# Kernel tuning notes

Measured on AMD Instinct MI355X. Metric: run time of the kernel, lower is better.

The kernel has to match this reference:

```python
import jax, jax.numpy as jnp
import numpy as np

DIM = 384
HEADS = 8
HD = DIM // HEADS
GAMMA = 0.5
EPS = 1e-6
BN_EPS = 1e-5
LN_EPS = 1e-5


def setup_inputs() -> dict:
    key = jax.random.key(0)
    ks = jax.random.split(key, 8)
    B, H, W = 8, 56, 56
    d = DIM
    w = lambda k, shp: (jax.random.normal(k, shp, jnp.float32) * 0.05)
    return {
        "x": jax.random.normal(ks[0], (B, d, H, W), jnp.float32),
        "bn1_w": jnp.ones((d,), jnp.float32), "bn1_b": jnp.zeros((d,), jnp.float32),
        "bn1_m": jnp.zeros((d,), jnp.float32), "bn1_v": jnp.ones((d,), jnp.float32),
        "cw1": w(ks[1], (d, d)), "cb1": jnp.zeros((d,), jnp.float32),
        "dw": w(ks[2], (d, 1, 3, 3)), "db": jnp.zeros((d,), jnp.float32),
        "bn2_w": jnp.ones((d,), jnp.float32), "bn2_b": jnp.zeros((d,), jnp.float32),
        "bn2_m": jnp.zeros((d,), jnp.float32), "bn2_v": jnp.ones((d,), jnp.float32),
        "cw2": w(ks[3], (d, d)), "cb2": jnp.zeros((d,), jnp.float32),
        "qkv_w": w(ks[4], (3 * d, d)),
        "proj_w": w(ks[5], (d, d)), "proj_b": jnp.zeros((d,), jnp.float32),
        "ln_w": jnp.ones((d,), jnp.float32), "ln_b": jnp.zeros((d,), jnp.float32),
        "mlp_w1": w(ks[6], (d, 4 * d)), "mlp_b1": jnp.zeros((4 * d,), jnp.float32),
        "mlp_w2": w(ks[7], (4 * d, d)), "mlp_b2": jnp.zeros((d,), jnp.float32),
    }


def _bn(t, w, b, m, v):
    # inference-mode BatchNorm2d over channel dim of NCHW
    s = w * jax.lax.rsqrt(v + BN_EPS)
    return (t - m[:, None, None]) * s[:, None, None] + b[:, None, None]


def _c1(t, w, b=None):
    # 1x1 conv as channel GEMM: (o,i) x (b,i,h,w) -> (b,o,h,w)
    y = jnp.einsum('oi,bihw->bohw', w, t)
    return y if b is None else y + b[:, None, None]


def _phi(t):
    return jnp.exp(GAMMA * (2.0 * t - t * t))


def reference(x, bn1_w, bn1_b, bn1_m, bn1_v, cw1, cb1, dw, db,
              bn2_w, bn2_b, bn2_m, bn2_v, cw2, cb2, qkv_w,
              proj_w, proj_b, ln_w, ln_b, mlp_w1, mlp_b1, mlp_w2, mlp_b2):
    B, C, H, W = x.shape
    N = H * W
    # conv_path with residual
    h = _bn(x, bn1_w, bn1_b, bn1_m, bn1_v)
    h = _c1(h, cw1, cb1)
    h = jax.lax.conv_general_dilated(h, dw, (1, 1), 'SAME',
                                     feature_group_count=DIM,
                                     dimension_numbers=('NCHW', 'OIHW', 'NCHW'))
    h = h + db[:, None, None]
    h = _bn(h, bn2_w, bn2_b, bn2_m, bn2_v)
    h = _c1(h, cw2, cb2)
    x1 = h + x
    # linear attention
    qkv = _c1(x1, qkv_w)  # (B, 3C, H, W)
    q, k, v = jnp.split(qkv, 3, axis=1)
    to_heads = lambda t: t.reshape(B, HEADS, HD, N).transpose(0, 1, 3, 2)  # (B,h,N,d)
    qp = _phi(to_heads(q))
    kp = _phi(to_heads(k))
    vv = to_heads(v)
    kv = jnp.einsum('bhnd,bhne->bhde', kp, vv)               # (B,h,d,d)
    z = 1.0 / (jnp.einsum('bhnd,bhd->bhn', qp, kp.sum(axis=2)) + EPS)
    out = jnp.einsum('bhnd,bhde->bhne', qp, kv) * z[..., None]  # (B,h,N,d)
    out = out.transpose(0, 1, 3, 2).reshape(B, C, H, W)
    out = _c1(out, proj_w, proj_b)
    x2 = x1 + out
    # LayerNorm + MLP over channels
    xf = x2.transpose(0, 2, 3, 1)  # (B,H,W,C)
    mu = xf.mean(-1, keepdims=True)
    var = xf.var(-1, keepdims=True)
    xn = (xf - mu) * jax.lax.rsqrt(var + LN_EPS) * ln_w + ln_b
    hmid = jax.nn.gelu(xn @ mlp_w1 + mlp_b1, approximate=False)
    mlp_out = hmid @ mlp_w2 + mlp_b2
    return x2 + mlp_out.transpose(0, 3, 1, 2)
```

## Files before the change

### kernel.cpp

```cpp
#include <hip/hip_runtime.h>

#define CDIM 384
#define NPIX 3136
#define BB 8
#define NROW (BB * NPIX)
#define HDIM 48
#define CMID 1536
#define BN_EPS 1e-5f
#define LN_EPS 1e-5f

typedef short s16x8 __attribute__((ext_vector_type(8)));
typedef float f32x4 __attribute__((ext_vector_type(4)));
typedef unsigned short u16;

__device__ __forceinline__ u16 f2bf(float f) {
    unsigned u = __builtin_bit_cast(unsigned, f);
    u = (u + 0x7FFFu + ((u >> 16) & 1u)) >> 16;
    return (u16)u;
}
__device__ __forceinline__ float bf2f(u16 h) {
    unsigned u = ((unsigned)h) << 16;
    return __builtin_bit_cast(float, u);
}
__device__ __forceinline__ float phi_act(float v) { return expf(0.5f * (2.f * v - v * v)); }
__device__ __forceinline__ float gelu_act(float v) { return 0.5f * v * (1.f + erff(v * 0.7071067811865476f)); }

#define GLL16(g, l) __builtin_amdgcn_global_load_lds( \
    (const __attribute__((address_space(1))) void*)(g), \
    (__attribute__((address_space(3))) void*)(l), 16, 0, 0)

template<int ACT, bool BIAS, bool RES, bool OBF, bool OF32, int TN, bool QKV>
__global__ __launch_bounds__(256) void gemm_mfma(
    const u16* __restrict__ A, const u16* __restrict__ Bw,
    u16* __restrict__ Cbf, u16* __restrict__ Cv, float* __restrict__ Cf,
    const float* __restrict__ res, const float* __restrict__ bias,
    int N, int K)
{
    constexpr int NFR = TN / 32;
    constexpr int TNw = TN / 2;
    constexpr int STR = TNw + 4;
    constexpr int KLOOP_U16 = 8192 + TN * 64;
    constexpr int STG_U16 = 4 * 64 * STR;
    constexpr int SMEM_N = KLOOP_U16 > STG_U16 ? KLOOP_U16 : STG_U16;
    __shared__ __align__(16) u16 smem[SMEM_N];
    u16* Asb = smem;
    u16* Bsb = smem + 8192;

    const int t  = threadIdx.x;
    const int wv = t >> 6, ln = t & 63;
    const int lm = ln & 15, lq = ln >> 4;
    const int wm = wv >> 1, wn = wv & 1;
    const int m0 = blockIdx.y << 7, n0 = blockIdx.x * TN;

    const u16* gA0 = A  + (long)(m0 + wv * 16 + lm) * K + lq * 8;
    const u16* gA1 = gA0 + (long)64 * K;
    const u16* gB0 = Bw + (long)(n0 + wv * 16 + lm) * K + lq * 8;
    const u16* gB1 = gB0 + (long)64 * K;

    f32x4 acc[4][NFR] = {};
    const int nk = K >> 5;

    GLL16(gA0, &Asb[wv * 512]);
    GLL16(gA1, &Asb[wv * 512 + 2048]);
    GLL16(gB0, &Bsb[wv * 512]);
    if constexpr (TN == 128) GLL16(gB1, &Bsb[wv * 512 + 2048]);

    for (int k = 0; k < nk; k++) {
        const int cur = k & 1;
        __syncthreads();
        if (k + 1 < nk) {
            const int nx = cur ^ 1;
            gA0 += 32; gA1 += 32; gB0 += 32;
            GLL16(gA0, &Asb[nx * 4096 + wv * 512]);
            GLL16(gA1, &Asb[nx * 4096 + wv * 512 + 2048]);
            GLL16(gB0, &Bsb[nx * TN * 32 + wv * 512]);
            if constexpr (TN == 128) { gB1 += 32; GLL16(gB1, &Bsb[nx * TN * 32 + wv * 512 + 2048]); }
        }
        s16x8 av[4], bv[NFR];
        #pragma unroll
        for (int mf = 0; mf < 4; mf++)
            av[mf] = *(const s16x8*)&Asb[cur * 4096 + (wm * 256 + mf * 64 + ln) * 8];
        #pragma unroll
        for (int nf = 0; nf < NFR; nf++)
            bv[nf] = *(const s16x8*)&Bsb[cur * TN * 32 + ((TN == 128 ? wn * 256 : wn * 128) + nf * 64 + ln) * 8];
        #pragma unroll
        for (int mf = 0; mf < 4; mf++)
            #pragma unroll
            for (int nf = 0; nf < NFR; nf++)
                acc[mf][nf] = __builtin_amdgcn_mfma_f32_16x16x32_bf16(
                    av[mf], bv[nf], acc[mf][nf], 0, 0, 0);
    }

    u16* obase = Cbf; int oldc = N; int ocol0 = n0;
    bool qk_phi = false;
    if constexpr (QKV) {
        if (n0 < 768) { obase = Cbf; oldc = 768; ocol0 = n0; qk_phi = true; }
        else          { obase = Cv;  oldc = 384; ocol0 = n0 - 768; }
    }

    if constexpr (OBF || QKV) {
        __syncthreads();
        u16* stg = smem + wv * (64 * STR);
        #pragma unroll
        for (int nf = 0; nf < NFR; nf++) {
            const int lc = nf * 16 + lm;
            const int gn = n0 + wn * TNw + lc;
            const float bval = BIAS ? bias[gn] : 0.f;
            #pragma unroll
            for (int mf = 0; mf < 4; mf++) {
                #pragma unroll
                for (int r = 0; r < 4; r++) {
                    const int lr = mf * 16 + lq * 4 + r;
                    float v = acc[mf][nf][r];
                    if (BIAS) v += bval;
                    if (ACT == 1) v = phi_act(v);
                    else if (ACT == 2) v = gelu_act(v);
                    if (QKV) { if (qk_phi) v = phi_act(v); }
                    const long off = (long)(m0 + wm * 64 + lr) * N + gn;
                    if (RES) v += res[off];
                    if (OF32) Cf[off] = v;
                    stg[lr * STR + lc] = f2bf(v);
                }
            }
        }
        __syncthreads();
        constexpr int CPR = TNw / 8;
        constexpr int RPI = 64 / CPR;
        const int cg = ln % CPR, rb = ln / CPR;
        #pragma unroll
        for (int it = 0; it < 64 / RPI; it++) {
            const int row = it * RPI + rb;
            const s16x8 vv = *(const s16x8*)&stg[row * STR + cg * 8];
            *(s16x8*)&obase[(long)(m0 + wm * 64 + row) * oldc + ocol0 + wn * TNw + cg * 8] = vv;
        }
    } else {
        #pragma unroll
        for (int nf = 0; nf < NFR; nf++) {
            const int gn = n0 + wn * TNw + nf * 16 + lm;
            const float bval = BIAS ? bias[gn] : 0.f;
            #pragma unroll
            for (int mf = 0; mf < 4; mf++) {
                const int gmb = m0 + wm * 64 + mf * 16 + lq * 4;
                #pragma unroll
                for (int r = 0; r < 4; r++) {
                    float v = acc[mf][nf][r];
                    if (BIAS) v += bval;
                    if (ACT == 1) v = phi_act(v);
                    else if (ACT == 2) v = gelu_act(v);
                    const long off = (long)(gmb + r) * N + gn;
                    if (RES) v += res[off];
                    Cf[off] = v;
                }
            }
        }
    }
}

__global__ __launch_bounds__(256) void nchw_to_nhwc(const float* __restrict__ x,
                                                    float* __restrict__ of,
                                                    u16* __restrict__ ob)
{
    __shared__ float tile[64 * 65];
    const int n0 = blockIdx.x << 6, c0 = blockIdx.y << 6, b = blockIdx.z;
    const int t = threadIdx.x;
    const float* ip = x + ((long)b * CDIM + c0) * NPIX + n0;
    for (int idx = t; idx < 4096; idx += 256) {
        const int cc = idx >> 6, nn = idx & 63;
        tile[cc * 65 + nn] = ip[(long)cc * NPIX + nn];
    }
    __syncthreads();
    for (int idx = t; idx < 4096; idx += 256) {
        const int nn = idx >> 6, cc = idx & 63;
        const float v = tile[cc * 65 + nn];
        const long o = ((long)b * NPIX + n0 + nn) * CDIM + c0 + cc;
        of[o] = v; ob[o] = f2bf(v);
    }
}

__global__ __launch_bounds__(256) void dwconv_nhwc(const u16* __restrict__ in,
                                                   const u16* __restrict__ wt,
                                                   u16* __restrict__ out)
{
    const long tid = (long)blockIdx.x * 256 + threadIdx.x;
    const int c8 = (int)(tid % 48);
    const int p  = (int)((tid / 48) % NPIX);
    const int b  = (int)(tid / (48LL * NPIX));
    const int y = p / 56, x = p % 56;
    const u16* base = in + (long)b * NPIX * CDIM + c8 * 8;
    float acc[8] = {};
    #pragma unroll
    for (int r = 0; r < 3; r++) {
        const int yy = y + r - 1;
        if ((unsigned)yy >= 56u) continue;
        #pragma unroll
        for (int s = 0; s < 3; s++) {
            const int xx = x + s - 1;
            if ((unsigned)xx >= 56u) continue;
            const s16x8 iv = *(const s16x8*)&base[(long)(yy * 56 + xx) * CDIM];
            const s16x8 wv = *(const s16x8*)&wt[(r * 3 + s) * CDIM + c8 * 8];
            #pragma unroll
            for (int j = 0; j < 8; j++)
                acc[j] = fmaf(bf2f((u16)iv[j]), bf2f((u16)wv[j]), acc[j]);
        }
    }
    s16x8 ov;
    #pragma unroll
    for (int j = 0; j < 8; j++) ov[j] = (short)f2bf(acc[j]);
    *(s16x8*)&out[((long)b * NPIX + p) * CDIM + c8 * 8] = ov;
}

__global__ __launch_bounds__(256) void attn_kv_k(const u16* __restrict__ qk,
                                                 const u16* __restrict__ vb,
                                                 float* __restrict__ kv,
                                                 float* __restrict__ ksum)
{
    const int sp = blockIdx.x, bh = blockIdx.y;
    const int b = bh >> 3, h = bh & 7;
    const u16* kbase = qk + (long)b * NPIX * 768 + 384 + h * HDIM;
    const u16* vbase = vb + (long)b * NPIX * CDIM + h * HDIM;
    __shared__ float kt[64 * 48];
    __shared__ float vt[64 * 48];
    const int t = threadIdx.x;
    const int dg = t >> 4, eg = t & 15;
    float acc[3][3] = {};
    float ks[3] = {};
    for (int tl = sp; tl < 49; tl += 8) {
        const int n0 = tl << 6;
        __syncthreads();
        for (int idx = t; idx < 3072; idx += 256) {
            const int nn = idx / 48, d = idx % 48;
            kt[idx] = bf2f(kbase[(long)(n0 + nn) * 768 + d]);
            vt[idx] = bf2f(vbase[(long)(n0 + nn) * CDIM + d]);
        }
        __syncthreads();
        for (int nn = 0; nn < 64; nn++) {
            float kvv[3], vvv[3];
            #pragma unroll
            for (int i = 0; i < 3; i++) kvv[i] = kt[nn * 48 + dg * 3 + i];
            #pragma unroll
            for (int j = 0; j < 3; j++) vvv[j] = vt[nn * 48 + eg * 3 + j];
            #pragma unroll
            for (int i = 0; i < 3; i++)
                #pragma unroll
                for (int j = 0; j < 3; j++)
                    acc[i][j] = fmaf(kvv[i], vvv[j], acc[i][j]);
            if (eg == 0) {
                #pragma unroll
                for (int i = 0; i < 3; i++) ks[i] += kvv[i];
            }
        }
    }
    float* kvp = kv + (long)bh * HDIM * HDIM;
    #pragma unroll
    for (int i = 0; i < 3; i++)
        #pragma unroll
        for (int j = 0; j < 3; j++)
            atomicAdd(&kvp[(dg * 3 + i) * HDIM + eg * 3 + j], acc[i][j]);
    if (eg == 0) {
        #pragma unroll
        for (int i = 0; i < 3; i++) atomicAdd(&ksum[bh * HDIM + dg * 3 + i], ks[i]);
    }
}

__global__ __launch_bounds__(256) void attn_out_k(const u16* __restrict__ qk,
                                                  const float* __restrict__ kv,
                                                  const float* __restrict__ ksum,
                                                  u16* __restrict__ outb)
{
    const int bh = blockIdx.y, b = bh >> 3, h = bh & 7;
    const int n0 = blockIdx.x << 6;
    const u16* qbase = qk + (long)b * NPIX * 768 + h * HDIM;
    __shared__ float qt[64 * 48];
    __shared__ float kvs[48 * 48];
    __shared__ float kss[48];
    const int t = threadIdx.x;
    for (int idx = t; idx < 3072; idx += 256) {
        const int nn = idx / 48, d = idx % 48;
        qt[idx] = bf2f(qbase[(long)(n0 + nn) * 768 + d]);
    }
    for (int idx = t; idx < 2304; idx += 256) kvs[idx] = kv[(long)bh * HDIM * HDIM + idx];
    if (t < 48) kss[t] = ksum[bh * HDIM + t];
    __syncthreads();
    const int nn = t & 63, eg = t >> 6;
    float a[12] = {};
    float dot = 0.f;
    for (int d = 0; d < 48; d++) {
        const float qd = qt[nn * 48 + d];
        dot = fmaf(qd, kss[d], dot);
        const float* kr = &kvs[d * 48 + eg * 12];
        #pragma unroll
        for (int e = 0; e < 12; e++) a[e] = fmaf(qd, kr[e], a[e]);
    }
    const float z = 1.f / (dot + 1e-6f);
    u16* op = outb + ((long)b * NPIX + n0 + nn) * CDIM + h * HDIM + eg * 12;
    #pragma unroll
    for (int e = 0; e < 12; e++) op[e] = f2bf(a[e] * z);
}

__global__ __launch_bounds__(256) void ln_k(const float* __restrict__ x2,
                                            const float* __restrict__ lw,
                                            const float* __restrict__ lb,
                                            u16* __restrict__ xn)
{
    const int row = blockIdx.x * 4 + (threadIdx.x >> 6);
    const int lane = threadIdx.x & 63;
    const float* rp = x2 + (long)row * CDIM;
    float2 v[3];
    float sum = 0.f, sq = 0.f;
    #pragma unroll
    for (int i = 0; i < 3; i++) {
        v[i] = *(const float2*)&rp[lane * 2 + i * 128];
        sum += v[i].x + v[i].y;
        sq = fmaf(v[i].x, v[i].x, fmaf(v[i].y, v[i].y, sq));
    }
    #pragma unroll
    for (int off = 1; off < 64; off <<= 1) {
        sum += __shfl_xor(sum, off);
        sq  += __shfl_xor(sq, off);
    }
    const float mu = sum * (1.f / CDIM);
    const float rs = rsqrtf(sq * (1.f / CDIM) - mu * mu + LN_EPS);
    u16* op = xn + (long)row * CDIM;
    #pragma unroll
    for (int i = 0; i < 3; i++) {
        const int c = lane * 2 + i * 128;
        op[c]     = f2bf((v[i].x - mu) * rs * lw[c] + lb[c]);
        op[c + 1] = f2bf((v[i].y - mu) * rs * lw[c + 1] + lb[c + 1]);
    }
}

__global__ __launch_bounds__(256) void final_out(const float* __restrict__ x2,
                                                 const float* __restrict__ mlp,
                                                 float* __restrict__ out)
{
    __shared__ float tile[64 * 65];
    const int n0 = blockIdx.x << 6, c0 = blockIdx.y << 6, b = blockIdx.z;
    const int t = threadIdx.x;
    for (int idx = t; idx < 4096; idx += 256) {
        const int nn = idx >> 6, cc = idx & 63;
        const long o = ((long)b * NPIX + n0 + nn) * CDIM + c0 + cc;
        tile[nn * 65 + cc] = x2[o] + mlp[o];
    }
    __syncthreads();
    float* op = out + ((long)b * CDIM + c0) * NPIX + n0;
    for (int idx = t; idx < 4096; idx += 256) {
        const int cc = idx >> 6, nn = idx & 63;
        op[(long)cc * NPIX + nn] = tile[nn * 65 + cc];
    }
}

__global__ void prep_bn_k(const float* __restrict__ w1, const float* __restrict__ b1,
                          const float* __restrict__ m1, const float* __restrict__ v1,
                          const float* __restrict__ w2, const float* __restrict__ b2,
                          const float* __restrict__ m2, const float* __restrict__ v2,
                          const float* __restrict__ db,
                          float* s1, float* t1, float* s2, float* t2)
{
    const int i = threadIdx.x;
    if (i < CDIM) {
        const float a = w1[i] * rsqrtf(v1[i] + BN_EPS);
        s1[i] = a; t1[i] = b1[i] - m1[i] * a;
        const float c = w2[i] * rsqrtf(v2[i] + BN_EPS);
        s2[i] = c; t2[i] = b2[i] - m2[i] * c + db[i] * c;
    }
}

__global__ __launch_bounds__(64) void prep_w_k(
    const float* __restrict__ cw1, const float* __restrict__ cb1,
    const float* __restrict__ cw2, const float* __restrict__ cb2,
    const float* __restrict__ s1, const float* __restrict__ t1,
    const float* __restrict__ s2, const float* __restrict__ t2,
    u16* __restrict__ w1e, float* __restrict__ b1e,
    u16* __restrict__ w2e, float* __restrict__ b2e)
{
    const int o = blockIdx.x;
    const bool sec = (o >= CDIM);
    const int oo = sec ? o - CDIM : o;
    const float* cw = sec ? cw2 : cw1;
    const float* cb = sec ? cb2 : cb1;
    const float* s  = sec ? s2  : s1;
    const float* tt = sec ? t2  : t1;
    u16* we = sec ? w2e : w1e;
    float* be = sec ? b2e : b1e;
    float part = 0.f;
    for (int i = threadIdx.x; i < CDIM; i += 64) {
        const float wv = cw[oo * CDIM + i];
        we[oo * CDIM + i] = f2bf(wv * s[i]);
        part += wv * tt[i];
    }
    for (int off = 32; off; off >>= 1) part += __shfl_down(part, off);
    if (threadIdx.x == 0) be[oo] = cb[oo] + part;
}

__global__ void cvt_k(const float* __restrict__ in, u16* __restrict__ out, int n)
{
    const int i = blockIdx.x * 256 + threadIdx.x;
    if (i < n) out[i] = f2bf(in[i]);
}

__global__ __launch_bounds__(256) void transcvt_k(const float* __restrict__ in,
                                                  u16* __restrict__ out, int R, int C)
{
    __shared__ float tile[64 * 65];
    const int c0 = blockIdx.x << 6, r0 = blockIdx.y << 6;
    const int t = threadIdx.x;
    for (int idx = t; idx < 4096; idx += 256) {
        const int rr = idx >> 6, cc = idx & 63;
        tile[rr * 65 + cc] = in[(long)(r0 + rr) * C + c0 + cc];
    }
    __syncthreads();
    for (int idx = t; idx < 4096; idx += 256) {
        const int cc = idx >> 6, rr = idx & 63;
        out[(long)(c0 + cc) * R + r0 + rr] = f2bf(tile[rr * 65 + cc]);
    }
}

__global__ void dwt_k(const float* __restrict__ dw, u16* __restrict__ o)
{
    const int i = blockIdx.x * 256 + threadIdx.x;
    if (i < 9 * CDIM) {
        const int c = i / 9, tap = i % 9;
        o[tap * CDIM + c] = f2bf(dw[i]);
    }
}

extern "C" void kernel_launch(void* const* d_in, const int* in_sizes, int n_in,
                              void* d_out, int out_size, void* d_ws, size_t ws_size,
                              hipStream_t stream)
{
    const float* x      = (const float*)d_in[0];
    const float* bn1_w  = (const float*)d_in[1];
    const float* bn1_b  = (const float*)d_in[2];
    const float* bn1_m  = (const float*)d_in[3];
    const float* bn1_v  = (const float*)d_in[4];
    const float* cw1    = (const float*)d_in[5];
    const float* cb1    = (const float*)d_in[6];
    const float* dwW    = (const float*)d_in[7];
    const float* db     = (const float*)d_in[8];
    const float* bn2_w  = (const float*)d_in[9];
    const float* bn2_b  = (const float*)d_in[10];
    const float* bn2_m  = (const float*)d_in[11];
    const float* bn2_v  = (const float*)d_in[12];
    const float* cw2    = (const float*)d_in[13];
    const float* cb2    = (const float*)d_in[14];
    const float* qkv_w  = (const float*)d_in[15];
    const float* proj_w = (const float*)d_in[16];
    const float* proj_b = (const float*)d_in[17];
    const float* ln_w   = (const float*)d_in[18];
    const float* ln_b   = (const float*)d_in[19];
    const float* mlp_w1 = (const float*)d_in[20];
    const float* mlp_b1 = (const float*)d_in[21];
    const float* mlp_w2 = (const float*)d_in[22];
    const float* mlp_b2 = (const float*)d_in[23];
    float* outF = (float*)d_out;

    const long S = (long)NROW * CDIM;
    float* wsf = (float*)d_ws;

    float* xh_f  = wsf;
    float* x2_f  = wsf;
    u16*   v_bf  = (u16*)wsf;
    float* x1_f  = wsf + S;
    u16*   hmid  = (u16*)(wsf + S);
    u16* ar   = (u16*)(wsf + 2 * S);
    u16* a0   = ar;
    u16* a1   = ar + S;
    u16* a2   = ar + 2 * S;
    float* mlp_f = (float*)(ar + S);
    u16* wtb   = (u16*)(wsf + 3 * S + S / 2);
    u16* w1e   = wtb;
    u16* w2e   = w1e + CDIM * CDIM;
    u16* qkvw  = w2e + CDIM * CDIM;
    u16* projw = qkvw + 1152 * CDIM;
    u16* mw1t  = projw + CDIM * CDIM;
    u16* mw2t  = mw1t + CMID * CDIM;
    u16* dwt   = mw2t + CDIM * CMID;
    float* fb  = (float*)(dwt + 9 * CDIM);
    float* b1e = fb;
    float* b2e = b1e + CDIM;
    float* s1  = b2e + CDIM;
    float* t1  = s1 + CDIM;
    float* s2  = t1 + CDIM;
    float* t2  = s2 + CDIM;
    float* kvb = t2 + CDIM;
    float* ksb = kvb + 64 * HDIM * HDIM;

    prep_bn_k<<<1, CDIM, 0, stream>>>(bn1_w, bn1_b, bn1_m, bn1_v,
                                      bn2_w, bn2_b, bn2_m, bn2_v, db, s1, t1, s2, t2);
    prep_w_k<<<2 * CDIM, 64, 0, stream>>>(cw1, cb1, cw2, cb2, s1, t1, s2, t2,
                                          w1e, b1e, w2e, b2e);
    cvt_k<<<(1152 * CDIM + 255) / 256, 256, 0, stream>>>(qkv_w, qkvw, 1152 * CDIM);
    cvt_k<<<(CDIM * CDIM + 255) / 256, 256, 0, stream>>>(proj_w, projw, CDIM * CDIM);
    transcvt_k<<<dim3(CMID / 64, CDIM / 64), 256, 0, stream>>>(mlp_w1, mw1t, CDIM, CMID);
    transcvt_k<<<dim3(CDIM / 64, CMID / 64), 256, 0, stream>>>(mlp_w2, mw2t, CMID, CDIM);
    dwt_k<<<(9 * CDIM + 255) / 256, 256, 0, stream>>>(dwW, dwt);

    nchw_to_nhwc<<<dim3(49, 6, 8), 256, 0, stream>>>(x, xh_f, a0);
    gemm_mfma<0, true, false, true, false, 64, false><<<dim3(6, 196), 256, 0, stream>>>(
        a0, w1e, a1, nullptr, nullptr, nullptr, b1e, CDIM, CDIM);
    dwconv_nhwc<<<(int)((long)BB * NPIX * 48 / 256), 256, 0, stream>>>(a1, dwt, a2);
    gemm_mfma<0, true, true, true, true, 64, false><<<dim3(6, 196), 256, 0, stream>>>(
        a2, w2e, a0, nullptr, x1_f, xh_f, b2e, CDIM, CDIM);
    gemm_mfma<0, false, false, true, false, 128, true><<<dim3(9, 196), 256, 0, stream>>>(
        a0, qkvw, a1, v_bf, nullptr, nullptr, nullptr, 1152, CDIM);
    hipMemsetAsync(kvb, 0, (size_t)(64 * HDIM * HDIM + 64 * HDIM) * sizeof(float), stream);
    attn_kv_k<<<dim3(8, 64), 256, 0, stream>>>(a1, v_bf, kvb, ksb);
    attn_out_k<<<dim3(49, 64), 256, 0, stream>>>(a1, kvb, ksb, a0);
    gemm_mfma<0, true, true, false, true, 64, false><<<dim3(6, 196), 256, 0, stream>>>(
        a0, projw, nullptr, nullptr, x2_f, x1_f, proj_b, CDIM, CDIM);
    ln_k<<<NROW / 4, 256, 0, stream>>>(x2_f, ln_w, ln_b, a0);
    const long RH = (long)NROW / 2;
    gemm_mfma<2, true, false, true, false, 128, false><<<dim3(12, 98), 256, 0, stream>>>(
        a0, mw1t, hmid, nullptr, nullptr, nullptr, mlp_b1, CMID, CDIM);
    gemm_mfma<0, true, false, false, true, 64, false><<<dim3(6, 98), 256, 0, stream>>>(
        hmid, mw2t, nullptr, nullptr, mlp_f, nullptr, mlp_b2, CDIM, CMID);
    gemm_mfma<2, true, false, true, false, 128, false><<<dim3(12, 98), 256, 0, stream>>>(
        a0 + RH * CDIM, mw1t, hmid, nullptr, nullptr, nullptr, mlp_b1, CMID, CDIM);
    gemm_mfma<0, true, false, false, true, 64, false><<<dim3(6, 98), 256, 0, stream>>>(
        hmid, mw2t, nullptr, nullptr, mlp_f + RH * CDIM, nullptr, mlp_b2, CDIM, CMID);
    final_out<<<dim3(49, 6, 8), 256, 0, stream>>>(x2_f, mlp_f, outF);
}
```

Before: 686.8 us.

## Move linear-attention KV and output contractions onto bf16 MFMA

Rewrites the attention K^T V reduction and the Q·KV output stage to use 16x16x32 bf16 MFMA instructions instead of scalar fp32 FMAs. The key sum is computed with an MFMA against a ones vector, and a new repack kernel converts KV and ksum to a padded, transposed bf16 layout. The output kernel stages results in LDS so it can issue coalesced vector stores. This cuts ALU work in the attention stages but adds a kernel launch and rounds KV to bf16, which may reduce accuracy.

```diff
diff --git a/kernel.cpp b/kernel.cpp
--- a/kernel.cpp
+++ b/kernel.cpp
@@ -209,7 +209,7 @@
     *(s16x8*)&out[((long)b * NPIX + p) * CDIM + c8 * 8] = ov;
 }
 
-__global__ __launch_bounds__(256) void attn_kv_k(const u16* __restrict__ qk,
+__global__ __launch_bounds__(256) void attn_kv_m(const u16* __restrict__ qk,
                                                  const u16* __restrict__ vb,
                                                  float* __restrict__ kv,
                                                  float* __restrict__ ksum)
@@ -218,83 +218,147 @@
     const int b = bh >> 3, h = bh & 7;
     const u16* kbase = qk + (long)b * NPIX * 768 + 384 + h * HDIM;
     const u16* vbase = vb + (long)b * NPIX * CDIM + h * HDIM;
-    __shared__ float kt[64 * 48];
-    __shared__ float vt[64 * 48];
+    __shared__ u16 kt[48 * 72];
+    __shared__ u16 vt[48 * 72];
     const int t = threadIdx.x;
-    const int dg = t >> 4, eg = t & 15;
-    float acc[3][3] = {};
-    float ks[3] = {};
+    const int wv = t >> 6, ln = t & 63, lm = ln & 15, lq = ln >> 4;
+
+    f32x4 acc[3] = {};
+    const s16x8 ones = {0x3F80, 0x3F80, 0x3F80, 0x3F80, 0x3F80, 0x3F80, 0x3F80, 0x3F80};
+
     for (int tl = sp; tl < 49; tl += 8) {
-        const int n0 = tl << 6;
+        const int nn0 = tl << 6;
         __syncthreads();
-        for (int idx = t; idx < 3072; idx += 256) {
-            const int nn = idx / 48, d = idx % 48;
-            kt[idx] = bf2f(kbase[(long)(n0 + nn) * 768 + d]);
-            vt[idx] = bf2f(vbase[(long)(n0 + nn) * CDIM + d]);
+        for (int idx = t; idx < 384; idx += 256) {
+            const int oct = idx >> 6, nn = idx & 63;
+            const s16x8 kvv = *(const s16x8*)&kbase[(long)(nn0 + nn) * 768 + oct * 8];
+            const s16x8 vvv = *(const s16x8*)&vbase[(long)(nn0 + nn) * CDIM + oct * 8];
+            #pragma unroll
+            for (int j = 0; j < 8; j++) {
+                kt[(oct * 8 + j) * 72 + nn] = (u16)kvv[j];
+                vt[(oct * 8 + j) * 72 + nn] = (u16)vvv[j];
+            }
         }
         __syncthreads();
-        for (int nn = 0; nn < 64; nn++) {
-            float kvv[3], vvv[3];
-            #pragma unroll
-            for (int i = 0; i < 3; i++) kvv[i] = kt[nn * 48 + dg * 3 + i];
-            #pragma unroll
-            for (int j = 0; j < 3; j++) vvv[j] = vt[nn * 48 + eg * 3 + j];
-            #pragma unroll
-            for (int i = 0; i < 3; i++)
+        #pragma unroll
+        for (int s = 0; s < 2; s++) {
+            if (wv < 3) {
+                const s16x8 av = *(const s16x8*)&kt[(wv * 16 + lm) * 72 + s * 32 + lq * 8];
                 #pragma unroll
-                for (int j = 0; j < 3; j++)
-                    acc[i][j] = fmaf(kvv[i], vvv[j], acc[i][j]);
-            if (eg == 0) {
+                for (int ef = 0; ef < 3; ef++) {
+                    const s16x8 bv = *(const s16x8*)&vt[(ef * 16 + lm) * 72 + s * 32 + lq * 8];
+                    acc[ef] = __builtin_amdgcn_mfma_f32_16x16x32_bf16(av, bv, acc[ef], 0, 0, 0);
+                }
+            } else {
                 #pragma unroll
-                for (int i = 0; i < 3; i++) ks[i] += kvv[i];
+                for (int mf = 0; mf < 3; mf++) {
+                    const s16x8 av = *(const s16x8*)&kt[(mf * 16 + lm) * 72 + s * 32 + lq * 8];
+                    acc[mf] = __builtin_amdgcn_mfma_f32_16x16x32_bf16(av, ones, acc[mf], 0, 0, 0);
+                }
             }
         }
     }
-    float* kvp = kv + (long)bh * HDIM * HDIM;
-    #pragma unroll
-    for (int i = 0; i < 3; i++)
-        #pragma unroll
-        for (int j = 0; j < 3; j++)
-            atomicAdd(&kvp[(dg * 3 + i) * HDIM + eg * 3 + j], acc[i][j]);
-    if (eg == 0) {
-        #pragma unroll
-        for (int i = 0; i < 3; i++) atomicAdd(&ksum[bh * HDIM + dg * 3 + i], ks[i]);
-    }
-}
-
-__global__ __launch_bounds__(256) void attn_out_k(const u16* __restrict__ qk,
-                                                  const float* __restrict__ kv,
-                                                  const float* __restrict__ ksum,
+    if (wv < 3) {
+        #pragma unroll
+        for (int ef = 0; ef < 3; ef++)
+            #pragma unroll
+            for (int r = 0; r < 4; r++)
+                atomicAdd(&kv[(long)bh * 2304 + (wv * 16 + lq * 4 + r) * 48 + ef * 16 + lm], acc[ef][r]);
+    } else {
+        if (lm == 0) {
+            #pragma unroll
+            for (int mf = 0; mf < 3; mf++)
+                #pragma unroll
+                for (int r = 0; r < 4; r++)
+                    atomicAdd(&ksum[bh * 48 + mf * 16 + lq * 4 + r], acc[mf][r]);
+        }
+    }
+}
+
+__global__ void repack_kv(const float* __restrict__ kvb, const float* __restrict__ ksb,
+                          u16* __restrict__ kvp, u16* __restrict__ ksp)
+{
+    const int bh = blockIdx.x, t = threadIdx.x;
+    for (int idx = t; idx < 3072; idx += 256) {
+        const int e = idx >> 6, d = idx & 63;
+        kvp[(long)bh * 3072 + idx] = (d < 48) ? f2bf(kvb[(long)bh * 2304 + d * 48 + e]) : (u16)0;
+    }
+    if (t < 64) ksp[bh * 64 + t] = (t < 48) ? f2bf(ksb[bh * 48 + t]) : (u16)0;
+}
+
+__global__ __launch_bounds__(256) void attn_out_m(const u16* __restrict__ qk,
+                                                  const u16* __restrict__ kvp,
+                                                  const u16* __restrict__ ksp,
                                                   u16* __restrict__ outb)
 {
-    const int bh = blockIdx.y, b = bh >> 3, h = bh & 7;
-    const int n0 = blockIdx.x << 6;
-    const u16* qbase = qk + (long)b * NPIX * 768 + h * HDIM;
-    __shared__ float qt[64 * 48];
-    __shared__ float kvs[48 * 48];
-    __shared__ float kss[48];
-    const int t = threadIdx.x;
-    for (int idx = t; idx < 3072; idx += 256) {
-        const int nn = idx / 48, d = idx % 48;
-        qt[idx] = bf2f(qbase[(long)(n0 + nn) * 768 + d]);
-    }
-    for (int idx = t; idx < 2304; idx += 256) kvs[idx] = kv[(long)bh * HDIM * HDIM + idx];
-    if (t < 48) kss[t] = ksum[bh * HDIM + t];
+    __shared__ __align__(16) u16 smem[4 * 7168];
+    const int mt = blockIdx.x, hh = blockIdx.y, b = blockIdx.z;
+    const int t = threadIdx.x, wv = t >> 6, ln = t & 63, lm = ln & 15, lq = ln >> 4;
+    const int h = hh * 4 + wv, bh = b * 8 + h;
+    u16* As = smem + wv * 7168;
+    u16* Bs = As + 4096;
+    const u16* Ab = qk + ((long)b * NPIX + mt * 64) * 768 + h * HDIM;
+    const u16* Bb = kvp + (long)bh * 3072;
+
+    #pragma unroll
+    for (int rg = 0; rg < 4; rg++)
+        #pragma unroll
+        for (int oh = 0; oh < 2; oh++)
+            GLL16(Ab + (long)(rg * 16 + lm) * 768 + oh * 32 + lq * 8, As + (rg * 128 + oh * 64) * 8);
+    #pragma unroll
+    for (int rg = 0; rg < 3; rg++)
+        #pragma unroll
+        for (int oh = 0; oh < 2; oh++)
+            GLL16(Bb + (rg * 16 + lm) * 64 + oh * 32 + lq * 8, Bs + (rg * 128 + oh * 64) * 8);
+
+    s16x8 kz[2];
+    kz[0] = *(const s16x8*)&ksp[bh * 64 + lq * 8];
+    kz[1] = *(const s16x8*)&ksp[bh * 64 + 32 + lq * 8];
+
     __syncthreads();
-    const int nn = t & 63, eg = t >> 6;
-    float a[12] = {};
-    float dot = 0.f;
-    for (int d = 0; d < 48; d++) {
-        const float qd = qt[nn * 48 + d];
-        dot = fmaf(qd, kss[d], dot);
-        const float* kr = &kvs[d * 48 + eg * 12];
-        #pragma unroll
-        for (int e = 0; e < 12; e++) a[e] = fmaf(qd, kr[e], a[e]);
-    }
-    const float z = 1.f / (dot + 1e-6f);
-    u16* op = outb + ((long)b * NPIX + n0 + nn) * CDIM + h * HDIM + eg * 12;
-    #pragma unroll
-    for (int e = 0; e < 12; e++) op[e] = f2bf(a[e] * z);
+
+    f32x4 acc[4][3] = {};
+    f32x4 accz[4] = {};
+    #pragma unroll
+    for (int s = 0; s < 2; s++) {
+        s16x8 av[4], bv[3];
+        #pragma unroll
+        for (int mf = 0; mf < 4; mf++)
+            av[mf] = *(const s16x8*)&As[(mf * 128 + s * 64 + ln) * 8];
+        #pragma unroll
+        for (int nf = 0; nf < 3; nf++)
+            bv[nf] = *(const s16x8*)&Bs[(nf * 128 + s * 64 + ln) * 8];
+        #pragma unroll
+        for (int mf = 0; mf < 4; mf++) {
+            #pragma unroll
+            for (int nf = 0; nf < 3; nf++)
+                acc[mf][nf] = __builtin_amdgcn_mfma_f32_16x16x32_bf16(av[mf], bv[nf], acc[mf][nf], 0, 0, 0);
+            accz[mf] = __builtin_amdgcn_mfma_f32_16x16x32_bf16(av[mf], kz[s], accz[mf], 0, 0, 0);
+        }
+    }
+
+    u16* stg = As;
+    #pragma unroll
+    for (int mf = 0; mf < 4; mf++) {
+        #pragma unroll
+        for (int r = 0; r < 4; r++) {
+            const float z = 1.f / (accz[mf][r] + 1e-6f);
+            const int row = mf * 16 + lq * 4 + r;
+            #pragma unroll
+            for (int nf = 0; nf < 3; nf++)
+                stg[row * 56 + nf * 16 + lm] = f2bf(acc[mf][nf][r] * z);
+        }
+    }
+    __syncthreads();
+
+    #pragma unroll
+    for (int it = 0; it < 6; it++) {
+        const int idx = it * 256 + t;
+        const int row = idx / 24, c = idx % 24;
+        const int sw = c / 6, c6 = c % 6;
+        const s16x8 vvv = *(const s16x8*)&smem[sw * 7168 + row * 56 + c6 * 8];
+        *(s16x8*)&outb[((long)b * NPIX + mt * 64 + row) * CDIM + hh * 192 + c * 8] = vvv;
+    }
 }
 
 __global__ __launch_bounds__(256) void ln_k(const float* __restrict__ x2,
@@ -484,6 +548,8 @@
     float* t2  = s2 + CDIM;
     float* kvb = t2 + CDIM;
     float* ksb = kvb + 64 * HDIM * HDIM;
+    u16*   kvp = (u16*)(ksb + 64 * HDIM);
+    u16*   ksp = kvp + 64 * 3072;
 
     prep_bn_k<<<1, CDIM, 0, stream>>>(bn1_w, bn1_b, bn1_m, bn1_v,
                                       bn2_w, bn2_b, bn2_m, bn2_v, db, s1, t1, s2, t2);
@@ -504,8 +570,9 @@
     gemm_mfma<0, false, false, true, false, 128, true><<<dim3(9, 196), 256, 0, stream>>>(
         a0, qkvw, a1, v_bf, nullptr, nullptr, nullptr, 1152, CDIM);
     hipMemsetAsync(kvb, 0, (size_t)(64 * HDIM * HDIM + 64 * HDIM) * sizeof(float), stream);
-    attn_kv_k<<<dim3(8, 64), 256, 0, stream>>>(a1, v_bf, kvb, ksb);
-    attn_out_k<<<dim3(49, 64), 256, 0, stream>>>(a1, kvb, ksb, a0);
+    attn_kv_m<<<dim3(8, 64), 256, 0, stream>>>(a1, v_bf, kvb, ksb);
+    repack_kv<<<64, 256, 0, stream>>>(kvb, ksb, kvp, ksp);
+    attn_out_m<<<dim3(49, 2, 8), 256, 0, stream>>>(a1, kvp, ksp, a0);
     gemm_mfma<0, true, true, false, true, 64, false><<<dim3(6, 196), 256, 0, stream>>>(
         a0, projw, nullptr, nullptr, x2_f, x1_f, proj_b, CDIM, CDIM);
     ln_k<<<NROW / 4, 256, 0, stream>>>(x2_f, ln_w, ln_b, a0);
```

Result: faster. 623.5 us (-9.2%).
